# Kernel tuning notes

Measured on AMD Instinct MI355X. Metric: run time of the kernel, lower is better.

## Reference

```python
import jax, jax.numpy as jnp
import numpy as np

N_QUBITS = 10
DEPTH = 3
KSIZE = 16
DILATION = 1
NFREQ = 8

I4 = np.eye(4, dtype=np.complex64)
XX4 = np.fliplr(np.eye(4)).astype(np.complex64)
YY4 = np.array([[0, 0, 0, -1], [0, 0, 1, 0], [0, 1, 0, 0], [-1, 0, 0, 0]], dtype=np.complex64)


def _u3(t, p, l):
    ct = jnp.cos(t / 2).astype(jnp.complex64)
    st = jnp.sin(t / 2).astype(jnp.complex64)
    ep, el = jnp.exp(1j * p), jnp.exp(1j * l)
    return jnp.stack([jnp.stack([ct, -el * st]), jnp.stack([ep * st, ep * el * ct])])


def _ising_zz(t):
    em, ep = jnp.exp(-0.5j * t), jnp.exp(0.5j * t)
    return jnp.diag(jnp.stack([em, ep, ep, em]))


def _ising_xx(t):
    return jnp.cos(t / 2) * I4 - 1j * jnp.sin(t / 2) * XX4


def _ising_yy(t):
    return jnp.cos(t / 2) * I4 - 1j * jnp.sin(t / 2) * YY4


def _cu3(t, p, l):
    # controlled-U3 (control = 1): deferred-measurement form of qml.cond(measure, U3)
    return jnp.eye(4, dtype=jnp.complex64).at[2:, 2:].set(_u3(t, p, l))


def _apply_1q(state, U, wire):
    s = jnp.moveaxis(state, 1 + wire, -1)
    if U.ndim == 3:  # per-sample gate (batched angles)
        s = jnp.einsum('bij,b...j->b...i', U, s)
    else:
        s = jnp.einsum('ij,...j->...i', U, s)
    return jnp.moveaxis(s, -1, 1 + wire)


def _apply_2q(state, U, w1, w2):
    s = jnp.moveaxis(state, (1 + w1, 1 + w2), (-2, -1))
    shp = s.shape
    s = s.reshape(shp[:-2] + (4,))
    s = jnp.einsum('ij,...j->...i', U, s)
    return jnp.moveaxis(s.reshape(shp), (-2, -1), (1 + w1, 1 + w2))


def _run_circuit(angles, freq_scale, conv_params, pool_params):
    Bm = angles.shape[0]
    state = jnp.zeros((Bm, 2 ** N_QUBITS), jnp.complex64).at[:, 0].set(1.0)
    state = state.reshape((Bm,) + (2,) * N_QUBITS)
    # frequency-matched encoding: RY(a) then RX(freq_scale * a), per-sample angles
    for i in range(N_QUBITS):
        a = angles[:, i]
        c = jnp.cos(a / 2).astype(jnp.complex64)
        s = jnp.sin(a / 2).astype(jnp.complex64)
        ry = jnp.stack([jnp.stack([c, -s], -1), jnp.stack([s, c], -1)], -2)
        state = _apply_1q(state, ry, i)
        b = freq_scale[i] * a
        cb = jnp.cos(b / 2).astype(jnp.complex64)
        sb = jnp.sin(b / 2).astype(jnp.complex64)
        rx = jnp.stack([jnp.stack([cb, -1j * sb], -1), jnp.stack([-1j * sb, cb], -1)], -2)
        state = _apply_1q(state, rx, i)
    wires = list(range(N_QUBITS))
    for layer in range(DEPTH):
        wp = conv_params[layer]
        nw = len(wires)
        for parity in (0, 1):
            for i2, w in enumerate(wires):
                if i2 % 2 == parity and i2 < nw - 1:
                    nxt = wires[i2 + 1]
                    state = _apply_1q(state, _u3(wp[i2, 0], wp[i2, 1], wp[i2, 2]), w)
                    state = _apply_1q(state, _u3(wp[i2 + 1, 3], wp[i2 + 1, 4], wp[i2 + 1, 5]), nxt)
                    state = _apply_2q(state, _ising_zz(wp[i2, 6]), w, nxt)
                    state = _apply_2q(state, _ising_yy(wp[i2, 7]), w, nxt)
                    state = _apply_2q(state, _ising_xx(wp[i2, 8]), w, nxt)
                    state = _apply_1q(state, _u3(wp[i2, 9], wp[i2, 10], wp[i2, 11]), w)
                    state = _apply_1q(state, _u3(wp[i2 + 1, 12], wp[i2 + 1, 13], wp[i2 + 1, 14]), nxt)
        pp = pool_params[layer]
        for i2, w in enumerate(wires):
            if i2 % 2 == 1:
                state = _apply_2q(state, _cu3(pp[i2 // 2, 0], pp[i2 // 2, 1], pp[i2 // 2, 2]), w, wires[i2 - 1])
        wires = wires[::2]
    p = jnp.abs(state) ** 2
    p = p.reshape(Bm, 2, -1).sum(-1)
    return p[:, 0] - p[:, 1]  # <Z_0>


def _forward(x, proj_w, proj_b, freq_scale, conv_params, pool_params, agg_weights):
    B, C, T = x.shape
    eff = DILATION * (KSIZE - 1)
    W = T - eff
    idx = jnp.arange(W)[:, None] + DILATION * jnp.arange(KSIZE)[None, :]  # [W,K]
    win = x[:, :, idx]  # [B,C,W,K]
    f = jnp.fft.rfft(win, axis=-1)[..., :NFREQ]  # [B,C,W,NF]
    feats = jnp.stack([jnp.log1p(jnp.abs(f)), jnp.angle(f) / jnp.pi], -1)  # [B,C,W,NF,2]
    feats = jnp.transpose(feats, (0, 2, 1, 3, 4)).reshape(B, W, -1)  # [B,W,C*NF*2]
    proj = jnp.tanh(feats @ proj_w.T + proj_b) * jnp.pi  # [B,W,n_qubits]
    ev = _run_circuit(proj.reshape(B * W, N_QUBITS), freq_scale, conv_params, pool_params)
    outs = ev.reshape(B, W)
    wts = jax.nn.softmax(agg_weights[:W])
    return (outs * wts[None, :]).sum(1)


def setup_inputs():
    key = jax.random.key(0)
    k = jax.random.split(key, 6)
    fft_dim = 22 * NFREQ * 2
    return {
        'x': jax.random.normal(k[0], (16, 22, 128), jnp.float32),
        'proj_w': jax.random.normal(k[1], (N_QUBITS, fft_dim), jnp.float32) / np.sqrt(fft_dim).astype(np.float32),
        'proj_b': jnp.zeros((N_QUBITS,), jnp.float32),
        'freq_scale': jnp.linspace(0.5, 3.0, N_QUBITS, dtype=jnp.float32),
        'conv_params': 0.1 * jax.random.normal(k[2], (DEPTH, N_QUBITS, 15), jnp.float32),
        'pool_params': 0.1 * jax.random.normal(k[3], (DEPTH, N_QUBITS // 2, 3), jnp.float32),
        'agg_weights': jnp.zeros((113,), jnp.float32),
    }


def reference(x, proj_w, proj_b, freq_scale, conv_params, pool_params, agg_weights):
    return _forward(x, proj_w, proj_b, freq_scale, conv_params, pool_params, agg_weights)
```

## Files before the change

kernel.cpp:

```cpp
#include <hip/hip_runtime.h>
#include <math.h>

#define NQ 10
#define NSTATE 1024
#define WW 113
#define BB 16
#define CC 22
#define KK 16
#define NF 8
#define FDIM 352
#define NS (BB*WW)
#define NGATE 23
#define SL(j) ((j) ^ (((j) >> 5) & 31))

__device__ __forceinline__ float2 cmul(float2 a, float2 b) {
    return make_float2(a.x*b.x - a.y*b.y, a.x*b.y + a.y*b.x);
}

__constant__ int G_KIND[NGATE]  = {0,0,0,0,0, 0,0,0,0, 1,1,1,1,1, 0,0,0,0, 1,1, 0,0, 1};
__constant__ int G_LAYER[NGATE] = {0,0,0,0,0, 0,0,0,0, 0,0,0,0,0, 1,1,1,1, 1,1, 2,2, 2};
__constant__ int G_IA[NGATE]    = {0,2,4,6,8, 1,3,5,7, 0,1,2,3,4, 0,2,1,3, 0,1, 0,1, 0};

__device__ void u3mat(float2* U, float th, float ph, float lm) {
    float ct, st, cp, sp, cl, sl;
    sincosf(th * 0.5f, &st, &ct);
    sincosf(ph, &sp, &cp);
    sincosf(lm, &sl, &cl);
    U[0] = make_float2(ct, 0.f);
    U[1] = make_float2(-cl * st, -sl * st);
    U[2] = make_float2(cp * st, sp * st);
    U[3] = make_float2((cp * cl - sp * sl) * ct, (sp * cl + cp * sl) * ct);
}

__device__ void mm4(float2* C, const float2* A, const float2* B) {
#pragma unroll
    for (int i = 0; i < 4; ++i)
#pragma unroll
        for (int j = 0; j < 4; ++j) {
            float2 acc = make_float2(0.f, 0.f);
#pragma unroll
            for (int k = 0; k < 4; ++k) {
                float2 p = cmul(A[i*4+k], B[k*4+j]);
                acc.x += p.x; acc.y += p.y;
            }
            C[i*4+j] = acc;
        }
}

__global__ __launch_bounds__(64) void prep_kernel(
    const float* __restrict__ conv,
    const float* __restrict__ pool,
    const float* __restrict__ aggw,
    float2* __restrict__ mats,
    float* __restrict__ wts,
    float* __restrict__ out)
{
    const int t = threadIdx.x;

    float a0 = (t < WW) ? aggw[t] : -1e30f;
    float a1 = (t + 64 < WW) ? aggw[t + 64] : -1e30f;
    float mx = fmaxf(a0, a1);
    for (int off = 32; off > 0; off >>= 1) mx = fmaxf(mx, __shfl_xor(mx, off));
    float e0 = (t < WW) ? expf(a0 - mx) : 0.f;
    float e1 = (t + 64 < WW) ? expf(a1 - mx) : 0.f;
    float es = e0 + e1;
    for (int off = 32; off > 0; off >>= 1) es += __shfl_xor(es, off);
    float inv = 1.0f / es;
    if (t < WW) wts[t] = e0 * inv;
    if (t + 64 < WW) wts[t + 64] = e1 * inv;
    if (t < BB) out[t] = 0.f;

    if (t >= NGATE) return;
    int kind = G_KIND[t], layer = G_LAYER[t], ia = G_IA[t];
    float2 F[16];
    if (kind == 0) {
        const float* wp = conv + layer * 150;
        float2 Uw0[4], Un0[4], Uw1[4], Un1[4];
        u3mat(Uw0, wp[ia*15+0], wp[ia*15+1], wp[ia*15+2]);
        u3mat(Un0, wp[(ia+1)*15+3], wp[(ia+1)*15+4], wp[(ia+1)*15+5]);
        u3mat(Uw1, wp[ia*15+9], wp[ia*15+10], wp[ia*15+11]);
        u3mat(Un1, wp[(ia+1)*15+12], wp[(ia+1)*15+13], wp[(ia+1)*15+14]);
        float2 Kpre[16], Kpost[16];
#pragma unroll
        for (int a = 0; a < 2; ++a)
#pragma unroll
        for (int b = 0; b < 2; ++b)
#pragma unroll
        for (int c = 0; c < 2; ++c)
#pragma unroll
        for (int d = 0; d < 2; ++d) {
            Kpre [(2*a+b)*4 + (2*c+d)] = cmul(Uw0[a*2+c], Un0[b*2+d]);
            Kpost[(2*a+b)*4 + (2*c+d)] = cmul(Uw1[a*2+c], Un1[b*2+d]);
        }
        float cz, sz, cy, sy, cx, sx;
        sincosf(wp[ia*15+6] * 0.5f, &sz, &cz);
        sincosf(wp[ia*15+7] * 0.5f, &sy, &cy);
        sincosf(wp[ia*15+8] * 0.5f, &sx, &cx);
        float2 Z[16], Y[16], X[16];
#pragma unroll
        for (int k = 0; k < 16; ++k) { Z[k] = make_float2(0,0); Y[k] = make_float2(0,0); X[k] = make_float2(0,0); }
        Z[0]  = make_float2(cz, -sz); Z[5]  = make_float2(cz, sz);
        Z[10] = make_float2(cz,  sz); Z[15] = make_float2(cz, -sz);
        Y[0] = Y[5] = Y[10] = Y[15] = make_float2(cy, 0);
        Y[0*4+3] = make_float2(0,  sy); Y[1*4+2] = make_float2(0, -sy);
        Y[2*4+1] = make_float2(0, -sy); Y[3*4+0] = make_float2(0,  sy);
        X[0] = X[5] = X[10] = X[15] = make_float2(cx, 0);
        X[0*4+3] = X[1*4+2] = X[2*4+1] = X[3*4+0] = make_float2(0, -sx);
        float2 T1[16], M[16], T2[16];
        mm4(T1, Y, Z);
        mm4(M, X, T1);
        mm4(T2, M, Kpre);
        mm4(F, Kpost, T2);
    } else {
        const float* pp = pool + layer * 15 + ia * 3;
        float2 U[4];
        u3mat(U, pp[0], pp[1], pp[2]);
#pragma unroll
        for (int k = 0; k < 16; ++k) F[k] = make_float2(0,0);
        F[0*4+0] = make_float2(1,0); F[1*4+1] = make_float2(1,0);
        F[2*4+2] = U[0]; F[2*4+3] = U[1];
        F[3*4+2] = U[2]; F[3*4+3] = U[3];
    }
#pragma unroll
    for (int k = 0; k < 16; ++k) mats[t*16 + k] = F[k];
}

template<int PW, int PN>
__device__ __forceinline__ void gate2q(float2* st, const float2* __restrict__ m, int tid)
{
    constexpr int PL = (PW < PN) ? PW : PN;
    constexpr int PH = (PW < PN) ? PN : PW;
    int t1   = ((tid >> PL) << (PL + 1)) | (tid & ((1 << PL) - 1));
    int base = ((t1  >> PH) << (PH + 1)) | (t1  & ((1 << PH) - 1));
    const int i0 = SL(base);
    const int i1 = SL(base | (1 << PN));
    const int i2 = SL(base | (1 << PW));
    const int i3 = SL(base | (1 << PW) | (1 << PN));
    float2 a[4];
    a[0] = st[i0]; a[1] = st[i1]; a[2] = st[i2]; a[3] = st[i3];
    float2 n[4];
#pragma unroll
    for (int g = 0; g < 4; ++g) {
        float accx = 0.f, accy = 0.f;
#pragma unroll
        for (int h = 0; h < 4; ++h) {
            float2 mm = m[g*4 + h];
            accx = fmaf(mm.x, a[h].x, accx);
            accx = fmaf(-mm.y, a[h].y, accx);
            accy = fmaf(mm.x, a[h].y, accy);
            accy = fmaf(mm.y, a[h].x, accy);
        }
        n[g] = make_float2(accx, accy);
    }
    st[i0] = n[0]; st[i1] = n[1]; st[i2] = n[2]; st[i3] = n[3];
}

__global__ __launch_bounds__(256) void fused_kernel(
    const float* __restrict__ x,
    const float* __restrict__ proj_w,
    const float* __restrict__ proj_b,
    const float* __restrict__ freq_scale,
    const float2* __restrict__ mats,
    const float* __restrict__ wts,
    float* __restrict__ out)
{
    const int s = blockIdx.x;
    const int b = s / WW, w = s % WW;
    const int tid = threadIdx.x;

    __shared__ float2 st[NSTATE];
    __shared__ float twre[16], twim[16];
    __shared__ float angs[NQ];
    __shared__ float2 vq[2 * NQ];
    __shared__ float part[4];

    float* win  = (float*)st;
    float* feat = (float*)st + 512;

    for (int e = tid; e < CC * KK; e += 256) {
        int c = e >> 4, n = e & 15;
        win[e] = x[b * (CC * 128) + c * 128 + w + n];
    }
    if (tid < 16) {
        float ang = -(float)M_PI * (float)tid / 8.0f;
        twre[tid] = cosf(ang);
        twim[tid] = sinf(ang);
    }
    __syncthreads();

    float fval = 0.f, fval2 = 0.f;
    if (tid < CC * NF) {
        int c = tid >> 3, k = tid & 7;
        float re = 0.f, im = 0.f;
#pragma unroll
        for (int n = 0; n < 16; ++n) {
            int m = (k * n) & 15;
            float xv = win[c * 16 + n];
            re += xv * twre[m];
            im += xv * twim[m];
        }
        fval  = log1pf(sqrtf(re * re + im * im));
        fval2 = atan2f(im, re) * (float)(1.0 / M_PI);
    }
    __syncthreads();
    if (tid < CC * NF) {
        int c = tid >> 3, k = tid & 7;
        feat[c * 16 + k * 2]     = fval;
        feat[c * 16 + k * 2 + 1] = fval2;
    }
    __syncthreads();

    {
        int v = tid >> 6, lane = tid & 63;
        for (int q = v; q < NQ; q += 4) {
            float acc = 0.f;
            for (int e = lane; e < FDIM; e += 64) acc += feat[e] * proj_w[q * FDIM + e];
            for (int off = 32; off > 0; off >>= 1) acc += __shfl_xor(acc, off);
            if (lane == 0) angs[q] = tanhf(acc + proj_b[q]) * (float)M_PI;
        }
    }
    __syncthreads();

    if (tid < NQ) {
        float a = angs[tid];
        float bf = freq_scale[tid] * a;
        float ca, sa, cb, sb;
        sincosf(a * 0.5f, &sa, &ca);
        sincosf(bf * 0.5f, &sb, &cb);
        vq[2 * tid]     = make_float2(cb * ca, -sb * sa);
        vq[2 * tid + 1] = make_float2(cb * sa, -sb * ca);
    }
    __syncthreads();

    for (int idx = tid; idx < NSTATE; idx += 256) {
        float r = 1.f, i = 0.f;
#pragma unroll
        for (int q = 0; q < NQ; ++q) {
            int bit = (idx >> (9 - q)) & 1;
            float2 vv = vq[2 * q + bit];
            float nr = r * vv.x - i * vv.y;
            float ni = r * vv.y + i * vv.x;
            r = nr; i = ni;
        }
        st[SL(idx)] = make_float2(r, i);
    }
    __syncthreads();

#define GATE(G, PW, PN) gate2q<PW, PN>(st, mats + (G)*16, tid); __syncthreads();
    GATE(0, 9, 8) GATE(1, 7, 6) GATE(2, 5, 4) GATE(3, 3, 2) GATE(4, 1, 0)
    GATE(5, 8, 7) GATE(6, 6, 5) GATE(7, 4, 3) GATE(8, 2, 1)
    GATE(9, 8, 9) GATE(10, 6, 7) GATE(11, 4, 5) GATE(12, 2, 3) GATE(13, 0, 1)
    GATE(14, 9, 7) GATE(15, 5, 3) GATE(16, 7, 5) GATE(17, 3, 1)
    GATE(18, 7, 9) GATE(19, 3, 5)
    GATE(20, 9, 5) GATE(21, 5, 1)
    GATE(22, 5, 9)
#undef GATE

    float local = 0.f;
    for (int idx = tid; idx < NSTATE; idx += 256) {
        float2 am = st[idx];
        float p = am.x * am.x + am.y * am.y;
        local += (idx < 512) ? p : -p;
    }
    for (int off = 32; off > 0; off >>= 1) local += __shfl_xor(local, off);
    if ((tid & 63) == 0) part[tid >> 6] = local;
    __syncthreads();
    if (tid == 0) {
        float ev = part[0] + part[1] + part[2] + part[3];
        atomicAdd(&out[b], ev * wts[w]);
    }
}

extern "C" void kernel_launch(void* const* d_in, const int* in_sizes, int n_in,
                              void* d_out, int out_size, void* d_ws, size_t ws_size,
                              hipStream_t stream)
{
    const float* x           = (const float*)d_in[0];
    const float* proj_w      = (const float*)d_in[1];
    const float* proj_b      = (const float*)d_in[2];
    const float* freq_scale  = (const float*)d_in[3];
    const float* conv_params = (const float*)d_in[4];
    const float* pool_params = (const float*)d_in[5];
    const float* aggw        = (const float*)d_in[6];
    float* out = (float*)d_out;

    float2* mats = (float2*)d_ws;
    float* wts   = (float*)d_ws + NGATE * 16 * 2;

    prep_kernel<<<1, 64, 0, stream>>>(conv_params, pool_params, aggw, mats, wts, out);
    fused_kernel<<<NS, 256, 0, stream>>>(x, proj_w, proj_b, freq_scale, mats, wts, out);
}
```

Baseline: 112.0 us.

## Simulate one sample per wavefront with register-resident state and LDS relayouts

Each wavefront now simulates a full 10-qubit state vector, 16 amplitudes per lane held in registers, instead of a whole 256-thread block sharing one state in LDS. Gates act on the four register-resident qubits, and LDS transposes swap which qubits live in registers between gate groups. This replaces 23 block-wide barriers and per-gate LDS round trips with a few wave-local relayouts that wait only on lgkmcnt. The cost is more serial work and register pressure per lane. Correctness relies on NS being divisible by 4 and on the in-wave LDS fence ordering being sufficient.

```diff
diff --git a/kernel.cpp b/kernel.cpp
--- a/kernel.cpp
+++ b/kernel.cpp
@@ -2,16 +2,19 @@
 #include <math.h>
 
 #define NQ 10
-#define NSTATE 1024
 #define WW 113
 #define BB 16
 #define CC 22
-#define KK 16
 #define NF 8
 #define FDIM 352
 #define NS (BB*WW)
 #define NGATE 23
-#define SL(j) ((j) ^ (((j) >> 5) & 31))
+#define SLOT(j) ((j) ^ (((j) >> 5) & 31))
+
+#define WAVE_FENCE() do { \
+    asm volatile("s_waitcnt lgkmcnt(0)" ::: "memory"); \
+    __builtin_amdgcn_sched_barrier(0); \
+} while (0)
 
 __device__ __forceinline__ float2 cmul(float2 a, float2 b) {
     return make_float2(a.x*b.x - a.y*b.y, a.x*b.y + a.y*b.x);
@@ -125,34 +128,71 @@
     for (int k = 0; k < 16; ++k) mats[t*16 + k] = F[k];
 }
 
-template<int PW, int PN>
-__device__ __forceinline__ void gate2q(float2* st, const float2* __restrict__ m, int tid)
-{
-    constexpr int PL = (PW < PN) ? PW : PN;
-    constexpr int PH = (PW < PN) ? PN : PW;
-    int t1   = ((tid >> PL) << (PL + 1)) | (tid & ((1 << PL) - 1));
-    int base = ((t1  >> PH) << (PH + 1)) | (t1  & ((1 << PH) - 1));
-    const int i0 = SL(base);
-    const int i1 = SL(base | (1 << PN));
-    const int i2 = SL(base | (1 << PW));
-    const int i3 = SL(base | (1 << PW) | (1 << PN));
-    float2 a[4];
-    a[0] = st[i0]; a[1] = st[i1]; a[2] = st[i2]; a[3] = st[i3];
-    float2 n[4];
-#pragma unroll
-    for (int g = 0; g < 4; ++g) {
-        float accx = 0.f, accy = 0.f;
-#pragma unroll
-        for (int h = 0; h < 4; ++h) {
-            float2 mm = m[g*4 + h];
-            accx = fmaf(mm.x, a[h].x, accx);
-            accx = fmaf(-mm.y, a[h].y, accx);
-            accy = fmaf(mm.x, a[h].y, accy);
-            accy = fmaf(mm.y, a[h].x, accy);
-        }
-        n[g] = make_float2(accx, accy);
-    }
-    st[i0] = n[0]; st[i1] = n[1]; st[i2] = n[2]; st[i3] = n[3];
+template<int B3,int B2,int B1,int B0>
+__device__ __forceinline__ int lanepart(int L) {
+    constexpr int rm = (1<<B3)|(1<<B2)|(1<<B1)|(1<<B0);
+    int idx = 0, lb = 5;
+#pragma unroll
+    for (int p = 9; p >= 0; --p)
+        if (!((rm >> p) & 1)) { idx |= ((L >> lb) & 1) << p; --lb; }
+    return idx;
+}
+
+template<int B3,int B2,int B1,int B0>
+__device__ __forceinline__ int rpart(int r) {
+    return (((r>>3)&1)<<B3) | (((r>>2)&1)<<B2) | (((r>>1)&1)<<B1) | ((r&1)<<B0);
+}
+
+template<int PA, int PB>
+__device__ __forceinline__ void rgate(float2* amp, const float2* __restrict__ m)
+{
+    constexpr int mask = (1<<PA) | (1<<PB);
+#pragma unroll
+    for (int base = 0; base < 16; ++base) {
+        if (base & mask) continue;
+        float2 a0 = amp[base];
+        float2 a1 = amp[base | (1<<PB)];
+        float2 a2 = amp[base | (1<<PA)];
+        float2 a3 = amp[base | mask];
+        float2 nn[4];
+#pragma unroll
+        for (int g = 0; g < 4; ++g) {
+            float2 m0 = m[g*4+0], m1 = m[g*4+1], m2 = m[g*4+2], m3 = m[g*4+3];
+            float rx, ry;
+            rx = m0.x*a0.x;            rx = fmaf(-m0.y, a0.y, rx);
+            rx = fmaf(m1.x, a1.x, rx); rx = fmaf(-m1.y, a1.y, rx);
+            rx = fmaf(m2.x, a2.x, rx); rx = fmaf(-m2.y, a2.y, rx);
+            rx = fmaf(m3.x, a3.x, rx); rx = fmaf(-m3.y, a3.y, rx);
+            ry = m0.x*a0.y;            ry = fmaf(m0.y, a0.x, ry);
+            ry = fmaf(m1.x, a1.y, ry); ry = fmaf(m1.y, a1.x, ry);
+            ry = fmaf(m2.x, a2.y, ry); ry = fmaf(m2.y, a2.x, ry);
+            ry = fmaf(m3.x, a3.y, ry); ry = fmaf(m3.y, a3.x, ry);
+            nn[g] = make_float2(rx, ry);
+        }
+        amp[base]           = nn[0];
+        amp[base | (1<<PB)] = nn[1];
+        amp[base | (1<<PA)] = nn[2];
+        amp[base | mask]    = nn[3];
+    }
+}
+
+template<int O3,int O2,int O1,int O0, int N3,int N2,int N1,int N0>
+__device__ __forceinline__ void relayout(float2* wst, float2* amp, int L)
+{
+    const int lo = lanepart<O3,O2,O1,O0>(L);
+#pragma unroll
+    for (int r = 0; r < 16; ++r) {
+        int idx = lo | rpart<O3,O2,O1,O0>(r);
+        wst[SLOT(idx)] = amp[r];
+    }
+    WAVE_FENCE();
+    const int ln = lanepart<N3,N2,N1,N0>(L);
+#pragma unroll
+    for (int r = 0; r < 16; ++r) {
+        int idx = ln | rpart<N3,N2,N1,N0>(r);
+        amp[r] = wst[SLOT(idx)];
+    }
+    WAVE_FENCE();
 }
 
 __global__ __launch_bounds__(256) void fused_kernel(
@@ -164,111 +204,140 @@
     const float* __restrict__ wts,
     float* __restrict__ out)
 {
-    const int s = blockIdx.x;
+    const int tid  = threadIdx.x;
+    const int wave = tid >> 6;
+    const int L    = tid & 63;
+    const int s = blockIdx.x * 4 + wave;
     const int b = s / WW, w = s % WW;
-    const int tid = threadIdx.x;
-
-    __shared__ float2 st[NSTATE];
-    __shared__ float twre[16], twim[16];
-    __shared__ float angs[NQ];
-    __shared__ float2 vq[2 * NQ];
-    __shared__ float part[4];
-
-    float* win  = (float*)st;
-    float* feat = (float*)st + 512;
-
-    for (int e = tid; e < CC * KK; e += 256) {
+
+    __shared__ float2 wst_all[4][1024];
+    float2* wst = wst_all[wave];
+
+    float*  win  = (float*)wst;
+    float*  feat = (float*)wst + 384;
+    float2* tw   = wst + 400;
+    float2* vq   = wst + 416;
+    float*  angs = (float*)wst + 880;
+
+    const float* xb = x + b * (CC * 128) + w;
+    for (int e = L; e < CC * 16; e += 64) {
         int c = e >> 4, n = e & 15;
-        win[e] = x[b * (CC * 128) + c * 128 + w + n];
-    }
-    if (tid < 16) {
-        float ang = -(float)M_PI * (float)tid / 8.0f;
-        twre[tid] = cosf(ang);
-        twim[tid] = sinf(ang);
-    }
-    __syncthreads();
-
-    float fval = 0.f, fval2 = 0.f;
-    if (tid < CC * NF) {
-        int c = tid >> 3, k = tid & 7;
+        win[e] = xb[c * 128 + n];
+    }
+    if (L < 16) {
+        float ang = -(float)M_PI * (float)L * 0.125f;
+        float sv, cv; sincosf(ang, &sv, &cv);
+        tw[L] = make_float2(cv, sv);
+    }
+    WAVE_FENCE();
+
+    for (int pidx = L; pidx < CC * NF; pidx += 64) {
+        int c = pidx >> 3, k = pidx & 7;
         float re = 0.f, im = 0.f;
 #pragma unroll
         for (int n = 0; n < 16; ++n) {
             int m = (k * n) & 15;
+            float2 t = tw[m];
             float xv = win[c * 16 + n];
-            re += xv * twre[m];
-            im += xv * twim[m];
-        }
-        fval  = log1pf(sqrtf(re * re + im * im));
-        fval2 = atan2f(im, re) * (float)(1.0 / M_PI);
-    }
-    __syncthreads();
-    if (tid < CC * NF) {
-        int c = tid >> 3, k = tid & 7;
-        feat[c * 16 + k * 2]     = fval;
-        feat[c * 16 + k * 2 + 1] = fval2;
-    }
-    __syncthreads();
+            re = fmaf(xv, t.x, re);
+            im = fmaf(xv, t.y, im);
+        }
+        feat[c * 16 + (k << 1)]     = log1pf(sqrtf(re * re + im * im));
+        feat[c * 16 + (k << 1) + 1] = atan2f(im, re) * (float)(1.0 / M_PI);
+    }
+    WAVE_FENCE();
 
     {
-        int v = tid >> 6, lane = tid & 63;
-        for (int q = v; q < NQ; q += 4) {
+        float fv[6];
+#pragma unroll
+        for (int k = 0; k < 6; ++k) {
+            int e = L + 64 * k;
+            fv[k] = (e < FDIM) ? feat[e] : 0.f;
+        }
+        for (int q = 0; q < NQ; ++q) {
+            const float* pw = proj_w + q * FDIM + L;
             float acc = 0.f;
-            for (int e = lane; e < FDIM; e += 64) acc += feat[e] * proj_w[q * FDIM + e];
+#pragma unroll
+            for (int k = 0; k < 6; ++k) {
+                float wv = (L + 64 * k < FDIM) ? pw[64 * k] : 0.f;
+                acc = fmaf(fv[k], wv, acc);
+            }
+#pragma unroll
             for (int off = 32; off > 0; off >>= 1) acc += __shfl_xor(acc, off);
-            if (lane == 0) angs[q] = tanhf(acc + proj_b[q]) * (float)M_PI;
-        }
-    }
-    __syncthreads();
-
-    if (tid < NQ) {
-        float a = angs[tid];
-        float bf = freq_scale[tid] * a;
+            if (L == 0) angs[q] = acc;
+        }
+    }
+    WAVE_FENCE();
+
+    if (L < NQ) {
+        float a = tanhf(angs[L] + proj_b[L]) * (float)M_PI;
+        float bf = freq_scale[L] * a;
         float ca, sa, cb, sb;
         sincosf(a * 0.5f, &sa, &ca);
         sincosf(bf * 0.5f, &sb, &cb);
-        vq[2 * tid]     = make_float2(cb * ca, -sb * sa);
-        vq[2 * tid + 1] = make_float2(cb * sa, -sb * ca);
-    }
-    __syncthreads();
-
-    for (int idx = tid; idx < NSTATE; idx += 256) {
-        float r = 1.f, i = 0.f;
-#pragma unroll
-        for (int q = 0; q < NQ; ++q) {
-            int bit = (idx >> (9 - q)) & 1;
-            float2 vv = vq[2 * q + bit];
-            float nr = r * vv.x - i * vv.y;
-            float ni = r * vv.y + i * vv.x;
-            r = nr; i = ni;
-        }
-        st[SL(idx)] = make_float2(r, i);
-    }
-    __syncthreads();
-
-#define GATE(G, PW, PN) gate2q<PW, PN>(st, mats + (G)*16, tid); __syncthreads();
-    GATE(0, 9, 8) GATE(1, 7, 6) GATE(2, 5, 4) GATE(3, 3, 2) GATE(4, 1, 0)
-    GATE(5, 8, 7) GATE(6, 6, 5) GATE(7, 4, 3) GATE(8, 2, 1)
-    GATE(9, 8, 9) GATE(10, 6, 7) GATE(11, 4, 5) GATE(12, 2, 3) GATE(13, 0, 1)
-    GATE(14, 9, 7) GATE(15, 5, 3) GATE(16, 7, 5) GATE(17, 3, 1)
-    GATE(18, 7, 9) GATE(19, 3, 5)
-    GATE(20, 9, 5) GATE(21, 5, 1)
-    GATE(22, 5, 9)
-#undef GATE
+        vq[2 * L]     = make_float2(cb * ca, -sb * sa);
+        vq[2 * L + 1] = make_float2(cb * sa, -sb * ca);
+    }
+    WAVE_FENCE();
+
+    float2 amp[16];
+    {
+        float2 pre = make_float2(1.f, 0.f);
+#pragma unroll
+        for (int p = 0; p < 6; ++p) {
+            float2 f = vq[2 * (9 - p) + ((L >> p) & 1)];
+            pre = cmul(pre, f);
+        }
+        float2 p98[4], p76[4];
+#pragma unroll
+        for (int i = 0; i < 4; ++i) {
+            p98[i] = cmul(vq[2 * 0 + (i >> 1)], vq[2 * 1 + (i & 1)]);
+            p76[i] = cmul(vq[2 * 2 + (i >> 1)], vq[2 * 3 + (i & 1)]);
+        }
+#pragma unroll
+        for (int r = 0; r < 16; ++r)
+            amp[r] = cmul(pre, cmul(p98[r >> 2], p76[r & 3]));
+    }
+    WAVE_FENCE();
+
+    rgate<3,2>(amp, mats + 0*16);
+    rgate<1,0>(amp, mats + 1*16);
+    rgate<2,1>(amp, mats + 5*16);
+    rgate<2,3>(amp, mats + 9*16);
+    relayout<9,8,7,6, 5,4,3,2>(wst, amp, L);
+    rgate<3,2>(amp, mats + 2*16);
+    rgate<1,0>(amp, mats + 3*16);
+    rgate<2,1>(amp, mats + 7*16);
+    relayout<5,4,3,2, 7,6,5,4>(wst, amp, L);
+    rgate<2,1>(amp, mats + 6*16);
+    rgate<2,3>(amp, mats + 10*16);
+    rgate<0,1>(amp, mats + 11*16);
+    relayout<7,6,5,4, 3,2,1,0>(wst, amp, L);
+    rgate<1,0>(amp, mats + 4*16);
+    rgate<2,1>(amp, mats + 8*16);
+    rgate<2,3>(amp, mats + 12*16);
+    rgate<0,1>(amp, mats + 13*16);
+    relayout<3,2,1,0, 9,7,5,3>(wst, amp, L);
+    rgate<3,2>(amp, mats + 14*16);
+    rgate<1,0>(amp, mats + 15*16);
+    rgate<2,1>(amp, mats + 16*16);
+    rgate<2,3>(amp, mats + 18*16);
+    relayout<9,7,5,3, 9,5,3,1>(wst, amp, L);
+    rgate<1,0>(amp, mats + 17*16);
+    rgate<1,2>(amp, mats + 19*16);
+    rgate<3,2>(amp, mats + 20*16);
+    rgate<2,0>(amp, mats + 21*16);
+    rgate<2,3>(amp, mats + 22*16);
 
     float local = 0.f;
-    for (int idx = tid; idx < NSTATE; idx += 256) {
-        float2 am = st[idx];
-        float p = am.x * am.x + am.y * am.y;
-        local += (idx < 512) ? p : -p;
-    }
+#pragma unroll
+    for (int r = 0; r < 16; ++r) {
+        float p = amp[r].x * amp[r].x + amp[r].y * amp[r].y;
+        local += (r & 8) ? -p : p;
+    }
+#pragma unroll
     for (int off = 32; off > 0; off >>= 1) local += __shfl_xor(local, off);
-    if ((tid & 63) == 0) part[tid >> 6] = local;
-    __syncthreads();
-    if (tid == 0) {
-        float ev = part[0] + part[1] + part[2] + part[3];
-        atomicAdd(&out[b], ev * wts[w]);
-    }
+    if (L == 0) atomicAdd(&out[b], local * wts[w]);
 }
 
 extern "C" void kernel_launch(void* const* d_in, const int* in_sizes, int n_in,
@@ -288,5 +357,5 @@
     float* wts   = (float*)d_ws + NGATE * 16 * 2;
 
     prep_kernel<<<1, 64, 0, stream>>>(conv_params, pool_params, aggw, mats, wts, out);
-    fused_kernel<<<NS, 256, 0, stream>>>(x, proj_w, proj_b, freq_scale, mats, wts, out);
-}
+    fused_kernel<<<NS / 4, 256, 0, stream>>>(x, proj_w, proj_b, freq_scale, mats, wts, out);
+}
```

Result: slower. 126.2 us (+12.6%).

## Hold statevector in registers across lanes with shuffle-based 2-qubit gates

Applied to the files above, without the earlier changes.

Replaces the shared-memory statevector (256 threads, one barrier per gate) with a register-resident layout. Each of 128 threads holds 8 amplitudes, three qubits map to register index, six to lane bits and one to wave index. Gates are applied with in-register math, cross-lane shuffles, or a single shared-memory exchange for the cross-wave gate, which removes most LDS traffic and barriers. It also halves the block size with launch bounds for higher occupancy, and restructures the projection dot product. In exchange the code carries much more per-gate index logic and higher register pressure.

```diff
diff --git a/kernel.cpp b/kernel.cpp
--- a/kernel.cpp
+++ b/kernel.cpp
@@ -2,19 +2,24 @@
 #include <math.h>
 
 #define NQ 10
-#define NSTATE 1024
 #define WW 113
 #define BB 16
 #define CC 22
-#define KK 16
 #define NF 8
 #define FDIM 352
 #define NS (BB*WW)
 #define NGATE 23
-#define SL(j) ((j) ^ (((j) >> 5) & 31))
-
-__device__ __forceinline__ float2 cmul(float2 a, float2 b) {
+
+
+__device__ __forceinline__ float2 cmulf(float2 a, float2 b) {
     return make_float2(a.x*b.x - a.y*b.y, a.x*b.y + a.y*b.x);
+}
+__device__ __forceinline__ void cmacf(float2& acc, float2 c, float2 v) {
+    acc.x = fmaf(c.x, v.x, acc.x); acc.x = fmaf(-c.y, v.y, acc.x);
+    acc.y = fmaf(c.x, v.y, acc.y); acc.y = fmaf(c.y, v.x, acc.y);
+}
+__device__ __forceinline__ float2 shflx(float2 v, int m) {
+    return make_float2(__shfl_xor(v.x, m, 64), __shfl_xor(v.y, m, 64));
 }
 
 __constant__ int G_KIND[NGATE]  = {0,0,0,0,0, 0,0,0,0, 1,1,1,1,1, 0,0,0,0, 1,1, 0,0, 1};
@@ -40,7 +45,7 @@
             float2 acc = make_float2(0.f, 0.f);
 #pragma unroll
             for (int k = 0; k < 4; ++k) {
-                float2 p = cmul(A[i*4+k], B[k*4+j]);
+                float2 p = cmulf(A[i*4+k], B[k*4+j]);
                 acc.x += p.x; acc.y += p.y;
             }
             C[i*4+j] = acc;
@@ -89,8 +94,8 @@
         for (int c = 0; c < 2; ++c)
 #pragma unroll
         for (int d = 0; d < 2; ++d) {
-            Kpre [(2*a+b)*4 + (2*c+d)] = cmul(Uw0[a*2+c], Un0[b*2+d]);
-            Kpost[(2*a+b)*4 + (2*c+d)] = cmul(Uw1[a*2+c], Un1[b*2+d]);
+            Kpre [(2*a+b)*4 + (2*c+d)] = cmulf(Uw0[a*2+c], Un0[b*2+d]);
+            Kpost[(2*a+b)*4 + (2*c+d)] = cmulf(Uw1[a*2+c], Un1[b*2+d]);
         }
         float cz, sz, cy, sy, cx, sx;
         sincosf(wp[ia*15+6] * 0.5f, &sz, &cz);
@@ -125,37 +130,160 @@
     for (int k = 0; k < 16; ++k) mats[t*16 + k] = F[k];
 }
 
-template<int PW, int PN>
-__device__ __forceinline__ void gate2q(float2* st, const float2* __restrict__ m, int tid)
-{
-    constexpr int PL = (PW < PN) ? PW : PN;
-    constexpr int PH = (PW < PN) ? PN : PW;
-    int t1   = ((tid >> PL) << (PL + 1)) | (tid & ((1 << PL) - 1));
-    int base = ((t1  >> PH) << (PH + 1)) | (t1  & ((1 << PH) - 1));
-    const int i0 = SL(base);
-    const int i1 = SL(base | (1 << PN));
-    const int i2 = SL(base | (1 << PW));
-    const int i3 = SL(base | (1 << PW) | (1 << PN));
-    float2 a[4];
-    a[0] = st[i0]; a[1] = st[i1]; a[2] = st[i2]; a[3] = st[i3];
-    float2 n[4];
-#pragma unroll
-    for (int g = 0; g < 4; ++g) {
-        float accx = 0.f, accy = 0.f;
-#pragma unroll
-        for (int h = 0; h < 4; ++h) {
-            float2 mm = m[g*4 + h];
-            accx = fmaf(mm.x, a[h].x, accx);
-            accx = fmaf(-mm.y, a[h].y, accx);
-            accy = fmaf(mm.x, a[h].y, accy);
-            accy = fmaf(mm.y, a[h].x, accy);
-        }
-        n[g] = make_float2(accx, accy);
-    }
-    st[i0] = n[0]; st[i1] = n[1]; st[i2] = n[2]; st[i3] = n[3];
-}
-
-__global__ __launch_bounds__(256) void fused_kernel(
+
+template<int RA, int RB>
+__device__ __forceinline__ void rr_conv(float2* amp, const float2* __restrict__ m)
+{
+    constexpr int mask = (1<<RA) | (1<<RB);
+#pragma unroll
+    for (int base = 0; base < 8; ++base) {
+        if (base & mask) continue;
+        float2 a0 = amp[base];
+        float2 a1 = amp[base | (1<<RB)];
+        float2 a2 = amp[base | (1<<RA)];
+        float2 a3 = amp[base | mask];
+        float2 n[4];
+#pragma unroll
+        for (int g = 0; g < 4; ++g) {
+            float2 acc = cmulf(m[g*4+0], a0);
+            cmacf(acc, m[g*4+1], a1);
+            cmacf(acc, m[g*4+2], a2);
+            cmacf(acc, m[g*4+3], a3);
+            n[g] = acc;
+        }
+        amp[base]           = n[0];
+        amp[base | (1<<RB)] = n[1];
+        amp[base | (1<<RA)] = n[2];
+        amp[base | mask]    = n[3];
+    }
+}
+
+template<int CR, int TR>
+__device__ __forceinline__ void rr_pool(float2* amp, const float2* __restrict__ m)
+{
+#pragma unroll
+    for (int base = 0; base < 8; ++base) {
+        if (!((base >> CR) & 1)) continue;
+        if ((base >> TR) & 1) continue;
+        float2 a2 = amp[base], a3 = amp[base | (1<<TR)];
+        float2 n2 = cmulf(m[10], a2); cmacf(n2, m[11], a3);
+        float2 n3 = cmulf(m[14], a2); cmacf(n3, m[15], a3);
+        amp[base] = n2; amp[base | (1<<TR)] = n3;
+    }
+}
+
+template<bool RIA>
+__device__ __forceinline__ constexpr int gidx(int rb, int lb) {
+    return RIA ? rb*2 + lb : lb*2 + rb;
+}
+
+template<int RP, int LPOS, bool RIA>
+__device__ __forceinline__ void rl_conv(float2* amp, const float2* __restrict__ m, int L)
+{
+    const int vL = (L >> LPOS) & 1;
+    constexpr int xm = 1 << LPOS;
+    float2 pamp[8];
+#pragma unroll
+    for (int r = 0; r < 8; ++r) pamp[r] = shflx(amp[r], xm);
+    float2 cOwn[2][2], cPar[2][2];
+#pragma unroll
+    for (int bo = 0; bo < 2; ++bo)
+#pragma unroll
+    for (int bi = 0; bi < 2; ++bi) {
+        cOwn[bo][bi] = vL ? m[gidx<RIA>(bo,1)*4 + gidx<RIA>(bi,1)]
+                          : m[gidx<RIA>(bo,0)*4 + gidx<RIA>(bi,0)];
+        cPar[bo][bi] = vL ? m[gidx<RIA>(bo,1)*4 + gidx<RIA>(bi,0)]
+                          : m[gidx<RIA>(bo,0)*4 + gidx<RIA>(bi,1)];
+    }
+    float2 out[8];
+#pragma unroll
+    for (int r = 0; r < 8; ++r) {
+        constexpr int RPC = RP;
+        const int bo = (r >> RPC) & 1;
+        const int r0 = r & ~(1 << RPC), r1 = r | (1 << RPC);
+        float2 acc = cmulf(bo ? cOwn[1][0] : cOwn[0][0], amp[r0]);
+        cmacf(acc, bo ? cOwn[1][1] : cOwn[0][1], amp[r1]);
+        cmacf(acc, bo ? cPar[1][0] : cPar[0][0], pamp[r0]);
+        cmacf(acc, bo ? cPar[1][1] : cPar[0][1], pamp[r1]);
+        out[r] = acc;
+    }
+#pragma unroll
+    for (int r = 0; r < 8; ++r) amp[r] = out[r];
+}
+
+template<int RP, int LPOS>
+__device__ __forceinline__ void rl_pool_clane(float2* amp, const float2* __restrict__ m, int L)
+{
+    const int vC = (L >> LPOS) & 1;
+    float2 out[8];
+#pragma unroll
+    for (int r = 0; r < 8; ++r) {
+        const int bo = (r >> RP) & 1;
+        const int r0 = r & ~(1 << RP), r1 = r | (1 << RP);
+        float2 acc = cmulf(bo ? m[14] : m[10], amp[r0]);
+        cmacf(acc, bo ? m[15] : m[11], amp[r1]);
+        out[r] = vC ? acc : amp[r];
+    }
+#pragma unroll
+    for (int r = 0; r < 8; ++r) amp[r] = out[r];
+}
+
+template<int RP, int LPOS>
+__device__ __forceinline__ void rl_pool_creg(float2* amp, const float2* __restrict__ m, int L)
+{
+    const int vT = (L >> LPOS) & 1;
+    constexpr int xm = 1 << LPOS;
+    float2 cO = vT ? m[15] : m[10];
+    float2 cP = vT ? m[14] : m[11];
+#pragma unroll
+    for (int r = 0; r < 8; ++r) {
+        if (!((r >> RP) & 1)) continue;
+        float2 p = shflx(amp[r], xm);
+        float2 nv = cmulf(cO, amp[r]); cmacf(nv, cP, p);
+        amp[r] = nv;
+    }
+}
+
+template<int LA, int LB>
+__device__ __forceinline__ void ll_conv(float2* amp, const float2* __restrict__ m, int L)
+{
+    const int vA = (L >> LA) & 1, vB = (L >> LB) & 1;
+    constexpr int ma = 1 << LA, mb = 1 << LB;
+#define SEL4(e0, e1, e2, e3) (vA ? (vB ? (e3) : (e2)) : (vB ? (e1) : (e0)))
+    float2 cS  = SEL4(m[0],  m[5],  m[10], m[15]);
+    float2 cA  = SEL4(m[2],  m[7],  m[8],  m[13]);
+    float2 cB  = SEL4(m[1],  m[4],  m[11], m[14]);
+    float2 cAB = SEL4(m[3],  m[6],  m[9],  m[12]);
+#undef SEL4
+    float2 out[8];
+#pragma unroll
+    for (int r = 0; r < 8; ++r) out[r] = cmulf(cS, amp[r]);
+#pragma unroll
+    for (int r = 0; r < 8; ++r) { float2 p = shflx(amp[r], ma); cmacf(out[r], cA, p); }
+#pragma unroll
+    for (int r = 0; r < 8; ++r) { float2 p = shflx(amp[r], mb); cmacf(out[r], cB, p); }
+#pragma unroll
+    for (int r = 0; r < 8; ++r) { float2 p = shflx(amp[r], ma^mb); cmacf(out[r], cAB, p); }
+#pragma unroll
+    for (int r = 0; r < 8; ++r) amp[r] = out[r];
+}
+
+template<int CA, int TB>
+__device__ __forceinline__ void ll_pool(float2* amp, const float2* __restrict__ m, int L)
+{
+    const int vC = (L >> CA) & 1, vT = (L >> TB) & 1;
+    constexpr int mb = 1 << TB;
+    float2 cO = vT ? m[15] : m[10];
+    float2 cP = vT ? m[14] : m[11];
+#pragma unroll
+    for (int r = 0; r < 8; ++r) {
+        float2 p = shflx(amp[r], mb);
+        float2 nv = cmulf(cO, amp[r]); cmacf(nv, cP, p);
+        amp[r] = vC ? nv : amp[r];
+    }
+}
+
+__global__ __launch_bounds__(128, 4) void fused_kernel(
     const float* __restrict__ x,
     const float* __restrict__ proj_w,
     const float* __restrict__ proj_b,
@@ -167,62 +295,68 @@
     const int s = blockIdx.x;
     const int b = s / WW, w = s % WW;
     const int tid = threadIdx.x;
-
-    __shared__ float2 st[NSTATE];
-    __shared__ float twre[16], twim[16];
-    __shared__ float angs[NQ];
-    __shared__ float2 vq[2 * NQ];
-    __shared__ float part[4];
-
-    float* win  = (float*)st;
-    float* feat = (float*)st + 512;
-
-    for (int e = tid; e < CC * KK; e += 256) {
+    const int wv  = tid >> 6;
+    const int L   = tid & 63;
+
+    __shared__ float2 buf[1024];
+    float*  win  = (float*)buf;
+    float*  feat = (float*)buf + 384;
+    float2* tw   = buf + 400;
+    float2* vq   = buf + 416;
+    float*  angs = (float*)buf + 880;
+
+    const float* xb = x + b * (CC * 128) + w;
+    for (int e = tid; e < CC * 16; e += 128) {
         int c = e >> 4, n = e & 15;
-        win[e] = x[b * (CC * 128) + c * 128 + w + n];
+        win[e] = xb[c * 128 + n];
     }
     if (tid < 16) {
-        float ang = -(float)M_PI * (float)tid / 8.0f;
-        twre[tid] = cosf(ang);
-        twim[tid] = sinf(ang);
+        float ang = -(float)M_PI * (float)tid * 0.125f;
+        float sv, cv; sincosf(ang, &sv, &cv);
+        tw[tid] = make_float2(cv, sv);
     }
     __syncthreads();
 
-    float fval = 0.f, fval2 = 0.f;
-    if (tid < CC * NF) {
-        int c = tid >> 3, k = tid & 7;
+    for (int pidx = tid; pidx < CC * NF; pidx += 128) {
+        int c = pidx >> 3, k = pidx & 7;
         float re = 0.f, im = 0.f;
 #pragma unroll
         for (int n = 0; n < 16; ++n) {
-            int m = (k * n) & 15;
+            int mm = (k * n) & 15;
+            float2 t = tw[mm];
             float xv = win[c * 16 + n];
-            re += xv * twre[m];
-            im += xv * twim[m];
-        }
-        fval  = log1pf(sqrtf(re * re + im * im));
-        fval2 = atan2f(im, re) * (float)(1.0 / M_PI);
+            re = fmaf(xv, t.x, re);
+            im = fmaf(xv, t.y, im);
+        }
+        feat[c * 16 + (k << 1)]     = log1pf(sqrtf(re * re + im * im));
+        feat[c * 16 + (k << 1) + 1] = atan2f(im, re) * (float)(1.0 / M_PI);
     }
     __syncthreads();
-    if (tid < CC * NF) {
-        int c = tid >> 3, k = tid & 7;
-        feat[c * 16 + k * 2]     = fval;
-        feat[c * 16 + k * 2 + 1] = fval2;
+
+    {
+        float fv[6];
+#pragma unroll
+        for (int k = 0; k < 6; ++k) {
+            int e = L + 64 * k;
+            fv[k] = (e < FDIM) ? feat[e] : 0.f;
+        }
+        for (int q = wv; q < NQ; q += 2) {
+            const float* pw = proj_w + q * FDIM + L;
+            float acc = 0.f;
+#pragma unroll
+            for (int k = 0; k < 6; ++k) {
+                float wvv = (L + 64 * k < FDIM) ? pw[64 * k] : 0.f;
+                acc = fmaf(fv[k], wvv, acc);
+            }
+#pragma unroll
+            for (int off = 32; off > 0; off >>= 1) acc += __shfl_xor(acc, off);
+            if (L == 0) angs[q] = acc;
+        }
     }
     __syncthreads();
 
-    {
-        int v = tid >> 6, lane = tid & 63;
-        for (int q = v; q < NQ; q += 4) {
-            float acc = 0.f;
-            for (int e = lane; e < FDIM; e += 64) acc += feat[e] * proj_w[q * FDIM + e];
-            for (int off = 32; off > 0; off >>= 1) acc += __shfl_xor(acc, off);
-            if (lane == 0) angs[q] = tanhf(acc + proj_b[q]) * (float)M_PI;
-        }
-    }
-    __syncthreads();
-
     if (tid < NQ) {
-        float a = angs[tid];
+        float a = tanhf(angs[tid] + proj_b[tid]) * (float)M_PI;
         float bf = freq_scale[tid] * a;
         float ca, sa, cb, sb;
         sincosf(a * 0.5f, &sa, &ca);
@@ -232,43 +366,102 @@
     }
     __syncthreads();
 
-    for (int idx = tid; idx < NSTATE; idx += 256) {
-        float r = 1.f, i = 0.f;
-#pragma unroll
-        for (int q = 0; q < NQ; ++q) {
-            int bit = (idx >> (9 - q)) & 1;
-            float2 vv = vq[2 * q + bit];
-            float nr = r * vv.x - i * vv.y;
-            float ni = r * vv.y + i * vv.x;
-            r = nr; i = ni;
-        }
-        st[SL(idx)] = make_float2(r, i);
-    }
-    __syncthreads();
-
-#define GATE(G, PW, PN) gate2q<PW, PN>(st, mats + (G)*16, tid); __syncthreads();
-    GATE(0, 9, 8) GATE(1, 7, 6) GATE(2, 5, 4) GATE(3, 3, 2) GATE(4, 1, 0)
-    GATE(5, 8, 7) GATE(6, 6, 5) GATE(7, 4, 3) GATE(8, 2, 1)
-    GATE(9, 8, 9) GATE(10, 6, 7) GATE(11, 4, 5) GATE(12, 2, 3) GATE(13, 0, 1)
-    GATE(14, 9, 7) GATE(15, 5, 3) GATE(16, 7, 5) GATE(17, 3, 1)
-    GATE(18, 7, 9) GATE(19, 3, 5)
-    GATE(20, 9, 5) GATE(21, 5, 1)
-    GATE(22, 5, 9)
-#undef GATE
+    float2 amp[8];
+    {
+        float2 pre = vq[2*0 + ((L>>5)&1)];
+        pre = cmulf(pre, vq[2*1 + ((L>>4)&1)]);
+        pre = cmulf(pre, vq[2*3 + ((L>>3)&1)]);
+        pre = cmulf(pre, vq[2*5 + ((L>>2)&1)]);
+        pre = cmulf(pre, vq[2*7 + ((L>>1)&1)]);
+        pre = cmulf(pre, vq[2*8 + (L&1)]);
+        pre = cmulf(pre, vq[2*9 + wv]);
+        float2 f2[2] = { vq[2*2], vq[2*2+1] };
+        float2 f4[2] = { vq[2*4], vq[2*4+1] };
+        float2 f6[2] = { vq[2*6], vq[2*6+1] };
+        float2 t46[4];
+#pragma unroll
+        for (int i = 0; i < 4; ++i) t46[i] = cmulf(f4[i>>1], f6[i&1]);
+#pragma unroll
+        for (int r = 0; r < 8; ++r)
+            amp[r] = cmulf(cmulf(pre, f2[(r>>2)&1]), t46[r & 3]);
+    }
+
+    ll_conv<5,4>(amp, mats + 0*16, L);
+    rl_conv<2,3,true >(amp, mats + 1*16, L);
+    rl_conv<1,2,true >(amp, mats + 2*16, L);
+    rl_conv<0,1,true >(amp, mats + 3*16, L);
+    {
+        const float2* m = mats + 4*16;
+        __syncthreads();
+#pragma unroll
+        for (int r = 0; r < 8; ++r) buf[wv*512 + r*64 + L] = amp[r];
+        __syncthreads();
+        const int vA = L & 1;
+        float2 cS, cL, cW, cLW;
+        if (wv == 0) {
+            cS  = vA ? m[10] : m[0];
+            cL  = vA ? m[8]  : m[2];
+            cW  = vA ? m[11] : m[1];
+            cLW = vA ? m[9]  : m[3];
+        } else {
+            cS  = vA ? m[15] : m[5];
+            cL  = vA ? m[13] : m[7];
+            cW  = vA ? m[14] : m[4];
+            cLW = vA ? m[12] : m[6];
+        }
+        float2 o[8];
+#pragma unroll
+        for (int r = 0; r < 8; ++r) {
+            float2 oW  = buf[(wv^1)*512 + r*64 + L];
+            float2 oWL = buf[(wv^1)*512 + r*64 + (L^1)];
+            float2 oL  = shflx(amp[r], 1);
+            float2 acc = cmulf(cS, amp[r]);
+            cmacf(acc, cL, oL);
+            cmacf(acc, cW, oW);
+            cmacf(acc, cLW, oWL);
+            o[r] = acc;
+        }
+#pragma unroll
+        for (int r = 0; r < 8; ++r) amp[r] = o[r];
+    }
+    rl_conv<2,4,false>(amp, mats + 5*16, L);
+    rl_conv<1,3,false>(amp, mats + 6*16, L);
+    rl_conv<0,2,false>(amp, mats + 7*16, L);
+    ll_conv<1,0>(amp, mats + 8*16, L);
+    ll_pool<4,5>(amp, mats + 9*16, L);
+    rl_pool_clane<2,3>(amp, mats + 10*16, L);
+    rl_pool_clane<1,2>(amp, mats + 11*16, L);
+    rl_pool_clane<0,1>(amp, mats + 12*16, L);
+    if (wv == 1) {
+        const float2* m = mats + 13*16;
+        const int vB = L & 1;
+        float2 cO = vB ? m[15] : m[10];
+        float2 cP = vB ? m[14] : m[11];
+#pragma unroll
+        for (int r = 0; r < 8; ++r) {
+            float2 p = shflx(amp[r], 1);
+            float2 nv = cmulf(cO, amp[r]); cmacf(nv, cP, p);
+            amp[r] = nv;
+        }
+    }
+    rl_conv<2,5,false>(amp, mats + 14*16, L);
+    rr_conv<1,0>(amp, mats + 15*16);
+    rr_conv<2,1>(amp, mats + 16*16);
+    rl_conv<0,0,true >(amp, mats + 17*16, L);
+    rl_pool_creg<2,5>(amp, mats + 18*16, L);
+    rr_pool<0,1>(amp, mats + 19*16);
+    rl_conv<1,5,false>(amp, mats + 20*16, L);
+    rl_conv<1,0,true >(amp, mats + 21*16, L);
+    rl_pool_creg<1,5>(amp, mats + 22*16, L);
 
     float local = 0.f;
-    for (int idx = tid; idx < NSTATE; idx += 256) {
-        float2 am = st[idx];
-        float p = am.x * am.x + am.y * am.y;
-        local += (idx < 512) ? p : -p;
-    }
+#pragma unroll
+    for (int r = 0; r < 8; ++r)
+        local += amp[r].x * amp[r].x + amp[r].y * amp[r].y;
+    local = ((L >> 5) & 1) ? -local : local;
+#pragma unroll
     for (int off = 32; off > 0; off >>= 1) local += __shfl_xor(local, off);
-    if ((tid & 63) == 0) part[tid >> 6] = local;
-    __syncthreads();
-    if (tid == 0) {
-        float ev = part[0] + part[1] + part[2] + part[3];
-        atomicAdd(&out[b], ev * wts[w]);
-    }
+    if (L == 0) atomicAdd(&out[b], local * wts[w]);
 }
 
 extern "C" void kernel_launch(void* const* d_in, const int* in_sizes, int n_in,
@@ -288,5 +481,5 @@
     float* wts   = (float*)d_ws + NGATE * 16 * 2;
 
     prep_kernel<<<1, 64, 0, stream>>>(conv_params, pool_params, aggw, mats, wts, out);
-    fused_kernel<<<NS, 256, 0, stream>>>(x, proj_w, proj_b, freq_scale, mats, wts, out);
-}
+    fused_kernel<<<NS, 128, 0, stream>>>(x, proj_w, proj_b, freq_scale, mats, wts, out);
+}
```

Result: slower. 136.9 us (+22.2%).
